# Performance work log

Hardware: AMD Instinct MI355X
Metric: run time of the kernel (lower is better)

Reference implementation:

```python
import jax, jax.numpy as jnp
import numpy as np

B, I, C, U, S = 256, 128, 1024, 32, 16  # batch, in_units, in_channels, num_units, unit_size
NUM_ITERS = 3

def setup_inputs() -> dict:
    key = jax.random.key(0)
    k1, k2 = jax.random.split(key)
    x = jax.random.normal(k1, (B, I, C), dtype=jnp.float32)
    W = jax.random.normal(k2, (1, C, U, S, I), dtype=jnp.float32)
    return {"x": x, "W": W}

def _squash(s):
    # s: (b, u, s); original squashes over dim=2 of (b,1,U,S,1), i.e. the num_units axis
    mag_sq = jnp.sum(s * s, axis=1, keepdims=True)
    mag = jnp.sqrt(mag_sq)
    return mag_sq / (1.0 + mag_sq) * (s / mag)

def reference(x, W):
    # x: (b, in_units, in_channels) -> (b, c, i)
    xT = jnp.swapaxes(x, 1, 2)
    # u_hat[b,c,u,s] = sum_i W[0,c,u,s,i] * xT[b,c,i]  (replaces torch.cat broadcast + matmul)
    u_hat = jnp.einsum('cusi,bci->bcus', W[0], xT)
    b_ij = jnp.zeros((1, C, U, 1), dtype=x.dtype)
    v_j = None
    for _ in range(NUM_ITERS):
        # softmax over axis 0 of size 1 -> all ones (faithful to original quirk)
        c_ij = jax.nn.softmax(b_ij, axis=0)
        s_j = jnp.einsum('cu,bcus->bus', c_ij[0, :, :, 0], u_hat)
        v_j = _squash(s_j)
        # agreement: mean over batch of <u_hat, v_j> along unit_size
        u_vj = jnp.einsum('bcus,bus->cu', u_hat, v_j) / B
        b_ij = b_ij + u_vj[None, :, :, None]
    return v_j[..., None]  # (b, num_units, unit_size, 1) == v_j.squeeze(1)
```

## Files before the change

kernel.cpp:

```cpp
#include <hip/hip_runtime.h>
#include <hip/hip_bf16.h>
#include <stdint.h>

#define B_DIM 256
#define I_DIM 128
#define C_DIM 1024
#define U_DIM 32
#define S_DIM 16
#define N_DIM 512
#define KC    (C_DIM * I_DIM)

typedef __bf16 bf16;
typedef __attribute__((ext_vector_type(8))) __bf16 bf16x8;
typedef __attribute__((ext_vector_type(4))) float f32x4;

__device__ __forceinline__ void async_copy16(const bf16* g, short* l) {
  __builtin_amdgcn_global_load_lds(
      (const __attribute__((address_space(1))) uint32_t*)g,
      (__attribute__((address_space(3))) uint32_t*)l, 16, 0, 0);
}

__global__ void __launch_bounds__(256)
transpose_cast(const float* __restrict__ x, bf16* __restrict__ xT) {
  __shared__ float tile[64][65];
  const int c0 = blockIdx.x * 64;
  const int i0 = blockIdx.y * 64;
  const int b  = blockIdx.z;
  const int t  = threadIdx.x;
  const int cl = t & 63;
  const int ib = t >> 6;
  const float* xb = x + (size_t)b * (I_DIM * C_DIM);
#pragma unroll
  for (int r = 0; r < 16; ++r) {
    const int il = r * 4 + ib;
    tile[il][cl] = xb[(size_t)(i0 + il) * C_DIM + c0 + cl];
  }
  __syncthreads();
  bf16* xTb = xT + (size_t)b * KC;
#pragma unroll
  for (int r = 0; r < 16; ++r) {
    const int clr = r * 4 + ib;
    xTb[(size_t)(c0 + clr) * I_DIM + i0 + cl] = (bf16)tile[cl][clr];
  }
}

__global__ void __launch_bounds__(512)
gemm_kernel(const bf16* __restrict__ xT, const float* __restrict__ W,
            float* __restrict__ sj) {
  __shared__ short Alds[B_DIM * I_DIM];
  const int tid  = threadIdx.x;
  const int lane = tid & 63;
  const int wave = tid >> 6;
  const int wm   = wave >> 1;
  const int wn   = wave & 1;
  const int l15  = lane & 15;
  const int lq   = lane >> 4;
  const int n0   = blockIdx.x * 128;
  const int c0   = blockIdx.y * 16;

  const int row_st   = tid >> 4;
  const int chunk_st = tid & 15;

  f32x4 acc[4][4] = {};

  for (int cc = 0; cc < 16; ++cc) {
    const int c = c0 + cc;
    __syncthreads();
#pragma unroll
    for (int r = 0; r < 8; ++r) {
      const int m    = r * 32 + row_st;
      const int csrc = chunk_st ^ (m & 15);
      const bf16* g  = xT + (size_t)m * KC + (size_t)c * I_DIM + csrc * 8;
      async_copy16(g, &Alds[m * I_DIM + chunk_st * 8]);
    }
    __syncthreads();

    const float* Wc = W + (size_t)c * (N_DIM * I_DIM);
#pragma unroll
    for (int ks = 0; ks < 4; ++ks) {
      const int i0 = ks * 32;
      bf16x8 a[4];
#pragma unroll
      for (int mt = 0; mt < 4; ++mt) {
        const int m  = wm * 64 + mt * 16 + l15;
        const int st = ((i0 >> 3) + lq) ^ l15;
        a[mt] = *(const bf16x8*)&Alds[m * I_DIM + st * 8];
      }
      bf16x8 b[4];
#pragma unroll
      for (int nt = 0; nt < 4; ++nt) {
        const int n = n0 + wn * 64 + nt * 16 + l15;
        const float* wp = Wc + (size_t)n * I_DIM + i0 + lq * 8;
        const float4 w0 = *(const float4*)(wp);
        const float4 w1 = *(const float4*)(wp + 4);
        bf16x8 bb;
        bb[0] = (bf16)w0.x; bb[1] = (bf16)w0.y;
        bb[2] = (bf16)w0.z; bb[3] = (bf16)w0.w;
        bb[4] = (bf16)w1.x; bb[5] = (bf16)w1.y;
        bb[6] = (bf16)w1.z; bb[7] = (bf16)w1.w;
        b[nt] = bb;
      }
#pragma unroll
      for (int mt = 0; mt < 4; ++mt)
#pragma unroll
        for (int nt = 0; nt < 4; ++nt)
          acc[mt][nt] = __builtin_amdgcn_mfma_f32_16x16x32_bf16(
              a[mt], b[nt], acc[mt][nt], 0, 0, 0);
    }
  }

#pragma unroll
  for (int mt = 0; mt < 4; ++mt) {
#pragma unroll
    for (int nt = 0; nt < 4; ++nt) {
      const int n = n0 + wn * 64 + nt * 16 + l15;
#pragma unroll
      for (int r = 0; r < 4; ++r) {
        const int brow = wm * 64 + mt * 16 + lq * 4 + r;
        atomicAdd(&sj[(size_t)brow * N_DIM + n], acc[mt][nt][r]);
      }
    }
  }
}

__global__ void __launch_bounds__(512)
squash_kernel(const float* __restrict__ sj, float* __restrict__ out) {
  __shared__ float sm[512];
  const int b = blockIdx.x;
  const int t = threadIdx.x;
  const float v = sj[(size_t)b * N_DIM + t];
  sm[t] = v * v;
  __syncthreads();
#pragma unroll
  for (int off = 256; off >= 16; off >>= 1) {
    if (t < off) sm[t] += sm[t + off];
    __syncthreads();
  }
  const float msq   = sm[t & 15];
  const float scale = sqrtf(msq) / (1.0f + msq);
  out[(size_t)b * N_DIM + t] = v * scale;
}

extern "C" void kernel_launch(void* const* d_in, const int* in_sizes, int n_in,
                              void* d_out, int out_size, void* d_ws, size_t ws_size,
                              hipStream_t stream) {
  const float* x = (const float*)d_in[0];
  const float* W = (const float*)d_in[1];
  float* out = (float*)d_out;

  bf16*  xT = (bf16*)d_ws;
  float* sj = (float*)((char*)d_ws + (size_t)B_DIM * KC * sizeof(bf16));

  hipMemsetAsync(sj, 0, (size_t)B_DIM * N_DIM * sizeof(float), stream);
  transpose_cast<<<dim3(C_DIM / 64, I_DIM / 64, B_DIM), 256, 0, stream>>>(x, xT);
  gemm_kernel<<<dim3(4, 64), 512, 0, stream>>>(xT, W, sj);
  squash_kernel<<<B_DIM, 512, 0, stream>>>(sj, out);
}
```

Baseline: 582.8 us.

## Vectorize transpose, halve GEMM N-tile, and register-prefetch W slices

The transpose kernel now reads float4 and writes packed bf16x4, where before it did scalar 4-byte loads and 2-byte stores. The GEMM block tile shrinks from 128 to 64 columns, doubling the grid to 512 blocks so more CUs are busy. It also adds a launch-bounds occupancy hint and double-buffers W fp32 loads in registers, so the next k-step's load overlaps the current MFMAs. The risks are that the A tile is now reloaded into LDS twice as often across blocks, and LDS-bank conflicts in the transposed read may rise.

```diff
diff --git a/kernel.cpp b/kernel.cpp
--- a/kernel.cpp
+++ b/kernel.cpp
@@ -5,12 +5,11 @@
 #define B_DIM 256
 #define I_DIM 128
 #define C_DIM 1024
-#define U_DIM 32
-#define S_DIM 16
 #define N_DIM 512
 #define KC    (C_DIM * I_DIM)
 
 typedef __bf16 bf16;
+typedef __attribute__((ext_vector_type(4))) __bf16 bf16x4;
 typedef __attribute__((ext_vector_type(8))) __bf16 bf16x8;
 typedef __attribute__((ext_vector_type(4))) float f32x4;
 
@@ -27,24 +26,31 @@
   const int i0 = blockIdx.y * 64;
   const int b  = blockIdx.z;
   const int t  = threadIdx.x;
-  const int cl = t & 63;
-  const int ib = t >> 6;
+  const int sub = t >> 4;
+  const int cg  = t & 15;
   const float* xb = x + (size_t)b * (I_DIM * C_DIM);
 #pragma unroll
-  for (int r = 0; r < 16; ++r) {
-    const int il = r * 4 + ib;
-    tile[il][cl] = xb[(size_t)(i0 + il) * C_DIM + c0 + cl];
+  for (int r = 0; r < 4; ++r) {
+    const int i = r * 16 + sub;
+    const float4 v = *(const float4*)&xb[(size_t)(i0 + i) * C_DIM + c0 + cg * 4];
+    tile[i][cg * 4 + 0] = v.x; tile[i][cg * 4 + 1] = v.y;
+    tile[i][cg * 4 + 2] = v.z; tile[i][cg * 4 + 3] = v.w;
   }
   __syncthreads();
   bf16* xTb = xT + (size_t)b * KC;
 #pragma unroll
-  for (int r = 0; r < 16; ++r) {
-    const int clr = r * 4 + ib;
-    xTb[(size_t)(c0 + clr) * I_DIM + i0 + cl] = (bf16)tile[cl][clr];
+  for (int r = 0; r < 4; ++r) {
+    const int c = r * 16 + sub;
+    bf16x4 o;
+    o[0] = (bf16)tile[cg * 4 + 0][c];
+    o[1] = (bf16)tile[cg * 4 + 1][c];
+    o[2] = (bf16)tile[cg * 4 + 2][c];
+    o[3] = (bf16)tile[cg * 4 + 3][c];
+    *(bf16x4*)&xTb[(size_t)(c0 + c) * I_DIM + i0 + cg * 4] = o;
   }
 }
 
-__global__ void __launch_bounds__(512)
+__global__ void __launch_bounds__(512, 4)
 gemm_kernel(const bf16* __restrict__ xT, const float* __restrict__ W,
             float* __restrict__ sj) {
   __shared__ short Alds[B_DIM * I_DIM];
@@ -55,17 +61,26 @@
   const int wn   = wave & 1;
   const int l15  = lane & 15;
   const int lq   = lane >> 4;
-  const int n0   = blockIdx.x * 128;
+  const int n0   = blockIdx.x * 64;
   const int c0   = blockIdx.y * 16;
-
   const int row_st   = tid >> 4;
   const int chunk_st = tid & 15;
 
-  f32x4 acc[4][4] = {};
+  f32x4 acc[4][2] = {};
 
   for (int cc = 0; cc < 16; ++cc) {
     const int c = c0 + cc;
+    const float* Wc = W + (size_t)c * (N_DIM * I_DIM);
     __syncthreads();
+
+    float4 wraw[2][2][2];
+#pragma unroll
+    for (int nt = 0; nt < 2; ++nt) {
+      const float* wp = Wc + (size_t)(n0 + wn * 32 + nt * 16 + l15) * I_DIM + lq * 8;
+      wraw[0][nt][0] = *(const float4*)wp;
+      wraw[0][nt][1] = *(const float4*)(wp + 4);
+    }
+
 #pragma unroll
     for (int r = 0; r < 8; ++r) {
       const int m    = r * 32 + row_st;
@@ -75,9 +90,18 @@
     }
     __syncthreads();
 
-    const float* Wc = W + (size_t)c * (N_DIM * I_DIM);
 #pragma unroll
     for (int ks = 0; ks < 4; ++ks) {
+      const int cur = ks & 1;
+      if (ks < 3) {
+        const int i0n = (ks + 1) * 32;
+#pragma unroll
+        for (int nt = 0; nt < 2; ++nt) {
+          const float* wp = Wc + (size_t)(n0 + wn * 32 + nt * 16 + l15) * I_DIM + i0n + lq * 8;
+          wraw[cur ^ 1][nt][0] = *(const float4*)wp;
+          wraw[cur ^ 1][nt][1] = *(const float4*)(wp + 4);
+        }
+      }
       const int i0 = ks * 32;
       bf16x8 a[4];
 #pragma unroll
@@ -86,13 +110,11 @@
         const int st = ((i0 >> 3) + lq) ^ l15;
         a[mt] = *(const bf16x8*)&Alds[m * I_DIM + st * 8];
       }
-      bf16x8 b[4];
+      bf16x8 b[2];
 #pragma unroll
-      for (int nt = 0; nt < 4; ++nt) {
-        const int n = n0 + wn * 64 + nt * 16 + l15;
-        const float* wp = Wc + (size_t)n * I_DIM + i0 + lq * 8;
-        const float4 w0 = *(const float4*)(wp);
-        const float4 w1 = *(const float4*)(wp + 4);
+      for (int nt = 0; nt < 2; ++nt) {
+        const float4 w0 = wraw[cur][nt][0];
+        const float4 w1 = wraw[cur][nt][1];
         bf16x8 bb;
         bb[0] = (bf16)w0.x; bb[1] = (bf16)w0.y;
         bb[2] = (bf16)w0.z; bb[3] = (bf16)w0.w;
@@ -103,7 +125,7 @@
 #pragma unroll
       for (int mt = 0; mt < 4; ++mt)
 #pragma unroll
-        for (int nt = 0; nt < 4; ++nt)
+        for (int nt = 0; nt < 2; ++nt)
           acc[mt][nt] = __builtin_amdgcn_mfma_f32_16x16x32_bf16(
               a[mt], b[nt], acc[mt][nt], 0, 0, 0);
     }
@@ -112,8 +134,8 @@
 #pragma unroll
   for (int mt = 0; mt < 4; ++mt) {
 #pragma unroll
-    for (int nt = 0; nt < 4; ++nt) {
-      const int n = n0 + wn * 64 + nt * 16 + l15;
+    for (int nt = 0; nt < 2; ++nt) {
+      const int n = n0 + wn * 32 + nt * 16 + l15;
 #pragma unroll
       for (int r = 0; r < 4; ++r) {
         const int brow = wm * 64 + mt * 16 + lq * 4 + r;
@@ -153,6 +175,6 @@
 
   hipMemsetAsync(sj, 0, (size_t)B_DIM * N_DIM * sizeof(float), stream);
   transpose_cast<<<dim3(C_DIM / 64, I_DIM / 64, B_DIM), 256, 0, stream>>>(x, xT);
-  gemm_kernel<<<dim3(4, 64), 512, 0, stream>>>(xT, W, sj);
+  gemm_kernel<<<dim3(8, 64), 512, 0, stream>>>(xT, W, sj);
   squash_kernel<<<B_DIM, 512, 0, stream>>>(sj, out);
 }
```

Result: faster. 550.2 us (-5.6%).
